# Performance work log

Measured on AMD Instinct MI355X. Metric: run time of the kernel, lower is better.

The kernel has to match this reference:

```python
import jax, jax.numpy as jnp
import numpy as np

N, E, IN_DIM, EMBED_DIM, HID_DIM = 10000, 320000, 128, 128, 64
NEG_SLOPE = 0.2


def setup_inputs() -> dict:
    key = jax.random.key(0)
    ks = jax.random.split(key, 7)
    x = jax.random.normal(ks[0], (N, IN_DIM), dtype=jnp.float32)
    edge_index = jax.random.randint(ks[1], (2, E), 0, N, dtype=jnp.int64)
    dense_w = jax.random.normal(ks[2], (IN_DIM, EMBED_DIM), dtype=jnp.float32) / np.sqrt(IN_DIM)
    dense_b = jnp.zeros((EMBED_DIM,), dtype=jnp.float32)
    gat_w = jax.random.normal(ks[3], (EMBED_DIM, HID_DIM), dtype=jnp.float32) / np.sqrt(EMBED_DIM)
    att_src = jax.random.normal(ks[4], (HID_DIM,), dtype=jnp.float32) * 0.1
    att_dst = jax.random.normal(ks[5], (HID_DIM,), dtype=jnp.float32) * 0.1
    gat_b = jnp.zeros((HID_DIM,), dtype=jnp.float32)
    return {"x": x, "edge_index": edge_index, "dense_w": dense_w, "dense_b": dense_b,
            "gat_w": gat_w, "att_src": att_src, "att_dst": att_dst, "gat_b": gat_b}


def reference(x, edge_index, dense_w, dense_b, gat_w, att_src, att_dst, gat_b):
    n = x.shape[0]
    # dense + relu
    h = jax.nn.relu(x @ dense_w + dense_b)            # [N, embed]
    # GATConv (heads=1): linear transform
    z = h @ gat_w                                     # [N, hid]
    # add self loops (PyG default)
    loops = jnp.arange(n, dtype=edge_index.dtype)
    src = jnp.concatenate([edge_index[0], loops])     # [E+N] message source j
    dst = jnp.concatenate([edge_index[1], loops])     # [E+N] message target i
    a_src = z @ att_src                               # [N]
    a_dst = z @ att_dst                               # [N]
    e = jax.nn.leaky_relu(a_src[src] + a_dst[dst], NEG_SLOPE)  # [E+N]
    # segment softmax over incoming edges of each target node
    m = jax.ops.segment_max(e, dst, num_segments=n)
    ex = jnp.exp(e - m[dst])
    denom = jax.ops.segment_sum(ex, dst, num_segments=n)
    alpha = ex / denom[dst]                           # [E+N]
    embed_x = jax.ops.segment_sum(alpha[:, None] * z[src], dst, num_segments=n) + gat_b  # [N, hid]
    # pairwise sigmoid similarity
    sim = jax.nn.sigmoid(embed_x @ embed_x.T)         # [N, N]
    return sim, embed_x
```

## Files before the change

kernel.cpp:

```cpp
#include <hip/hip_runtime.h>
#include <math.h>

#define N_NODES 10000
#define E_EDGES 320000
#define IN_DIM 128
#define EMB 128
#define HID 64
#define NEG_SLOPE 0.2f

typedef __attribute__((ext_vector_type(8))) short short8;
typedef __attribute__((ext_vector_type(4))) float floatx4;

__device__ __forceinline__ short f2bf(float f) {
    unsigned u = __float_as_uint(f);
    unsigned r = u + 0x7fffu + ((u >> 16) & 1u);
    return (short)(r >> 16);
}

__global__ __launch_bounds__(128) void dense_gat_kernel(
    const float* __restrict__ x, const float* __restrict__ dw,
    const float* __restrict__ db, const float* __restrict__ gw,
    const float* __restrict__ asv, const float* __restrict__ adv,
    float* __restrict__ z, float* __restrict__ a_src, float* __restrict__ a_dst)
{
    __shared__ float xs[8][IN_DIM];
    __shared__ float hs[8][EMB];
    const int t = threadIdx.x;
    const int row0 = blockIdx.x * 8;

    #pragma unroll
    for (int r = 0; r < 8; ++r)
        xs[r][t] = x[(row0 + r) * IN_DIM + t];
    __syncthreads();

    float acc[8];
    {
        const float bias = db[t];
        #pragma unroll
        for (int r = 0; r < 8; ++r) acc[r] = bias;
    }
    for (int j = 0; j < IN_DIM; ++j) {
        const float wj = dw[j * EMB + t];
        #pragma unroll
        for (int r = 0; r < 8; ++r) acc[r] = fmaf(xs[r][j], wj, acc[r]);
    }
    #pragma unroll
    for (int r = 0; r < 8; ++r) hs[r][t] = fmaxf(acc[r], 0.f);
    __syncthreads();

    if (t < HID) {
        float zacc[8];
        #pragma unroll
        for (int r = 0; r < 8; ++r) zacc[r] = 0.f;
        for (int k = 0; k < EMB; ++k) {
            const float g = gw[k * HID + t];
            #pragma unroll
            for (int r = 0; r < 8; ++r) zacc[r] = fmaf(hs[r][k], g, zacc[r]);
        }
        const float as = asv[t], ad = adv[t];
        #pragma unroll
        for (int r = 0; r < 8; ++r) {
            const int row = row0 + r;
            z[row * HID + t] = zacc[r];
            float ps = zacc[r] * as;
            float pd = zacc[r] * ad;
            #pragma unroll
            for (int off = 32; off > 0; off >>= 1) {
                ps += __shfl_down(ps, off, 64);
                pd += __shfl_down(pd, off, 64);
            }
            if (t == 0) { a_src[row] = ps; a_dst[row] = pd; }
        }
    }
}

__global__ __launch_bounds__(256) void count_kernel(
    const int* __restrict__ ei, int* __restrict__ cnt)
{
    const int e = blockIdx.x * blockDim.x + threadIdx.x;
    const int total = E_EDGES + N_NODES;
    if (e >= total) return;
    int s, d;
    if (e < E_EDGES) { s = ei[e]; d = ei[E_EDGES + e]; }
    else             { s = d = e - E_EDGES; }
    if ((unsigned)s >= N_NODES || (unsigned)d >= N_NODES) return;
    atomicAdd(&cnt[d], 1);
}

__global__ __launch_bounds__(256) void scan_kernel(
    const int* __restrict__ cnt, int* __restrict__ offs, int* __restrict__ cursor)
{
    __shared__ int part[256];
    const int t = threadIdx.x;
    const int base = t * 40;
    int vals[40];
    int local = 0;
    #pragma unroll
    for (int i = 0; i < 40; ++i) {
        const int idx = base + i;
        const int c = (idx < N_NODES) ? cnt[idx] : 0;
        vals[i] = c;
        local += c;
    }
    part[t] = local;
    __syncthreads();
    for (int off = 1; off < 256; off <<= 1) {
        const int v = (t >= off) ? part[t - off] : 0;
        __syncthreads();
        part[t] += v;
        __syncthreads();
    }
    int running = (t == 0) ? 0 : part[t - 1];
    #pragma unroll
    for (int i = 0; i < 40; ++i) {
        const int idx = base + i;
        if (idx < N_NODES) { offs[idx] = running; cursor[idx] = running; }
        running += vals[i];
    }
    if (t == 255) offs[N_NODES] = running;
}

__global__ __launch_bounds__(256) void scatter_kernel(
    const int* __restrict__ ei, const float* __restrict__ a_src,
    const float* __restrict__ a_dst, int* __restrict__ cursor,
    int* __restrict__ srcs, float* __restrict__ ew)
{
    const int e = blockIdx.x * blockDim.x + threadIdx.x;
    const int total = E_EDGES + N_NODES;
    if (e >= total) return;
    int s, d;
    if (e < E_EDGES) { s = ei[e]; d = ei[E_EDGES + e]; }
    else             { s = d = e - E_EDGES; }
    if ((unsigned)s >= N_NODES || (unsigned)d >= N_NODES) return;
    float v = a_src[s] + a_dst[d];
    v = (v > 0.f) ? v : NEG_SLOPE * v;
    const float w = __expf(v);
    const int pos = atomicAdd(&cursor[d], 1);
    srcs[pos] = s;
    ew[pos]   = w;
}

__global__ __launch_bounds__(256) void aggregate_kernel(
    const int* __restrict__ offs, const int* __restrict__ srcs,
    const float* __restrict__ ew, const float* __restrict__ z,
    const float* __restrict__ gb, float* __restrict__ emb)
{
    const int wid  = (blockIdx.x * blockDim.x + threadIdx.x) >> 6;
    const int lane = threadIdx.x & 63;
    if (wid >= N_NODES) return;
    const int beg = offs[wid], end = offs[wid + 1];
    float acc = 0.f, sw = 0.f;
    for (int i = beg; i < end; ++i) {
        const int s   = srcs[i];
        const float w = ew[i];
        acc = fmaf(w, z[s * HID + lane], acc);
        sw += w;
    }
    emb[wid * HID + lane] = acc / sw + gb[lane];
}

__global__ __launch_bounds__(256) void sim_kernel(
    const float* __restrict__ emb, float* __restrict__ sim)
{
    const int t    = threadIdx.x;
    const int lane = t & 63;
    const int wave = t >> 6;
    const int wm   = (wave >> 1) * 64;
    const int wn   = (wave & 1) * 64;
    const int rowBase = blockIdx.y * 128 + wm;
    const int colBase = blockIdx.x * 128 + wn;
    const int l15  = lane & 15;
    const int quad = lane >> 4;

    short8 afrag[4][2], bfrag[4][2];
    #pragma unroll
    for (int ti = 0; ti < 4; ++ti) {
        int r = rowBase + ti * 16 + l15; if (r > N_NODES - 1) r = N_NODES - 1;
        int c = colBase + ti * 16 + l15; if (c > N_NODES - 1) c = N_NODES - 1;
        #pragma unroll
        for (int ks = 0; ks < 2; ++ks) {
            const floatx4* pa = (const floatx4*)&emb[r * HID + ks * 32 + quad * 8];
            const floatx4* pb = (const floatx4*)&emb[c * HID + ks * 32 + quad * 8];
            const floatx4 a0 = pa[0], a1 = pa[1];
            const floatx4 b0 = pb[0], b1 = pb[1];
            short8 af, bf;
            #pragma unroll
            for (int j = 0; j < 4; ++j) { af[j] = f2bf(a0[j]); af[4 + j] = f2bf(a1[j]); }
            #pragma unroll
            for (int j = 0; j < 4; ++j) { bf[j] = f2bf(b0[j]); bf[4 + j] = f2bf(b1[j]); }
            afrag[ti][ks] = af;
            bfrag[ti][ks] = bf;
        }
    }

    floatx4 acc[4][4];
    const floatx4 zero = {0.f, 0.f, 0.f, 0.f};
    #pragma unroll
    for (int ti = 0; ti < 4; ++ti)
        #pragma unroll
        for (int tj = 0; tj < 4; ++tj) acc[ti][tj] = zero;

    #pragma unroll
    for (int ti = 0; ti < 4; ++ti)
        #pragma unroll
        for (int tj = 0; tj < 4; ++tj) {
            acc[ti][tj] = __builtin_amdgcn_mfma_f32_16x16x32_bf16(
                afrag[ti][0], bfrag[tj][0], acc[ti][tj], 0, 0, 0);
            acc[ti][tj] = __builtin_amdgcn_mfma_f32_16x16x32_bf16(
                afrag[ti][1], bfrag[tj][1], acc[ti][tj], 0, 0, 0);
        }

    #pragma unroll
    for (int ti = 0; ti < 4; ++ti) {
        #pragma unroll
        for (int reg = 0; reg < 4; ++reg) {
            const int gr = rowBase + ti * 16 + quad * 4 + reg;
            if (gr >= N_NODES) continue;
            const size_t rowoff = (size_t)gr * N_NODES;
            #pragma unroll
            for (int tj = 0; tj < 4; ++tj) {
                const int gc = colBase + tj * 16 + l15;
                if (gc < N_NODES) {
                    const float v = acc[ti][tj][reg];
                    sim[rowoff + gc] = __builtin_amdgcn_rcpf(1.f + __expf(-v));
                }
            }
        }
    }
}

extern "C" void kernel_launch(void* const* d_in, const int* in_sizes, int n_in,
                              void* d_out, int out_size, void* d_ws, size_t ws_size,
                              hipStream_t stream)
{
    const float* x   = (const float*)d_in[0];
    const int*   ei  = (const int*)d_in[1];
    const float* dw  = (const float*)d_in[2];
    const float* db  = (const float*)d_in[3];
    const float* gw  = (const float*)d_in[4];
    const float* asv = (const float*)d_in[5];
    const float* adv = (const float*)d_in[6];
    const float* gb  = (const float*)d_in[7];

    float* out = (float*)d_out;
    float* sim = out;
    float* emb = out + (size_t)N_NODES * N_NODES;

    const size_t need = 1350001u * sizeof(float);
    float* ws = (ws_size >= need) ? (float*)d_ws : out;
    float* z      = ws;
    float* a_src  = ws + 640000;
    float* a_dst  = ws + 650000;
    int*   cnt    = (int*)(ws + 660000);
    int*   offs   = (int*)(ws + 670000);
    int*   cursor = (int*)(ws + 680001);
    int*   srcs   = (int*)(ws + 690001);
    float* ew     = ws + 1020001;

    hipMemsetAsync(cnt, 0, N_NODES * sizeof(int), stream);

    dense_gat_kernel<<<N_NODES / 8, 128, 0, stream>>>(x, dw, db, gw, asv, adv,
                                                      z, a_src, a_dst);

    const int total_edges = E_EDGES + N_NODES;
    const int eb = (total_edges + 255) / 256;
    count_kernel<<<eb, 256, 0, stream>>>(ei, cnt);
    scan_kernel<<<1, 256, 0, stream>>>(cnt, offs, cursor);
    scatter_kernel<<<eb, 256, 0, stream>>>(ei, a_src, a_dst, cursor, srcs, ew);
    aggregate_kernel<<<(N_NODES * 64 + 255) / 256, 256, 0, stream>>>(
        offs, srcs, ew, z, gb, emb);

    dim3 grid((N_NODES + 127) / 128, (N_NODES + 127) / 128);
    sim_kernel<<<grid, 256, 0, stream>>>(emb, sim);
}
```

Baseline: 581.0 us.

## Stage sim tiles in LDS as bf16 and rebalance dense GAT kernel

Measured after the change: 563.3 us. 3.0% less time.

```diff
diff --git a/kernel.cpp b/kernel.cpp
--- a/kernel.cpp
+++ b/kernel.cpp
@@ -9,6 +9,7 @@
 #define NEG_SLOPE 0.2f
 
 typedef __attribute__((ext_vector_type(8))) short short8;
+typedef __attribute__((ext_vector_type(4))) short short4_t;
 typedef __attribute__((ext_vector_type(4))) float floatx4;
 
 __device__ __forceinline__ short f2bf(float f) {
@@ -17,61 +18,71 @@
     return (short)(r >> 16);
 }
 
-__global__ __launch_bounds__(128) void dense_gat_kernel(
+__global__ __launch_bounds__(256) void dense_gat_kernel(
     const float* __restrict__ x, const float* __restrict__ dw,
     const float* __restrict__ db, const float* __restrict__ gw,
-    const float* __restrict__ asv, const float* __restrict__ adv,
-    float* __restrict__ z, float* __restrict__ a_src, float* __restrict__ a_dst)
-{
-    __shared__ float xs[8][IN_DIM];
-    __shared__ float hs[8][EMB];
+    float* __restrict__ z)
+{
+    __shared__ float xs[16][IN_DIM];
+    __shared__ float hs[16][EMB];
     const int t = threadIdx.x;
-    const int row0 = blockIdx.x * 8;
-
-    #pragma unroll
-    for (int r = 0; r < 8; ++r)
-        xs[r][t] = x[(row0 + r) * IN_DIM + t];
-    __syncthreads();
-
-    float acc[8];
+    const int row0 = blockIdx.x * 16;
+
+    #pragma unroll
+    for (int r = 0; r < 2; ++r) {
+        const int idx = t + r * 256;
+        const int row = idx >> 5, c4 = idx & 31;
+        *(floatx4*)&xs[row][c4 * 4] =
+            *(const floatx4*)&x[(row0 + row) * IN_DIM + c4 * 4];
+    }
+    __syncthreads();
+
     {
-        const float bias = db[t];
+        const int col = t & 127, rb = (t >> 7) * 8;
+        float acc[8];
+        const float bias = db[col];
         #pragma unroll
         for (int r = 0; r < 8; ++r) acc[r] = bias;
-    }
-    for (int j = 0; j < IN_DIM; ++j) {
-        const float wj = dw[j * EMB + t];
-        #pragma unroll
-        for (int r = 0; r < 8; ++r) acc[r] = fmaf(xs[r][j], wj, acc[r]);
-    }
-    #pragma unroll
-    for (int r = 0; r < 8; ++r) hs[r][t] = fmaxf(acc[r], 0.f);
-    __syncthreads();
-
-    if (t < HID) {
-        float zacc[8];
-        #pragma unroll
-        for (int r = 0; r < 8; ++r) zacc[r] = 0.f;
+        for (int j = 0; j < IN_DIM; ++j) {
+            const float wj = dw[j * EMB + col];
+            #pragma unroll
+            for (int r = 0; r < 8; ++r) acc[r] = fmaf(xs[rb + r][j], wj, acc[r]);
+        }
+        #pragma unroll
+        for (int r = 0; r < 8; ++r) hs[rb + r][col] = fmaxf(acc[r], 0.f);
+    }
+    __syncthreads();
+
+    {
+        const int col = t & 63, rb = (t >> 6) * 4;
+        float acc[4] = {0.f, 0.f, 0.f, 0.f};
         for (int k = 0; k < EMB; ++k) {
-            const float g = gw[k * HID + t];
+            const float g = gw[k * HID + col];
             #pragma unroll
-            for (int r = 0; r < 8; ++r) zacc[r] = fmaf(hs[r][k], g, zacc[r]);
-        }
-        const float as = asv[t], ad = adv[t];
-        #pragma unroll
-        for (int r = 0; r < 8; ++r) {
-            const int row = row0 + r;
-            z[row * HID + t] = zacc[r];
-            float ps = zacc[r] * as;
-            float pd = zacc[r] * ad;
-            #pragma unroll
-            for (int off = 32; off > 0; off >>= 1) {
-                ps += __shfl_down(ps, off, 64);
-                pd += __shfl_down(pd, off, 64);
-            }
-            if (t == 0) { a_src[row] = ps; a_dst[row] = pd; }
-        }
-    }
+            for (int r = 0; r < 4; ++r) acc[r] = fmaf(hs[rb + r][k], g, acc[r]);
+        }
+        #pragma unroll
+        for (int r = 0; r < 4; ++r) z[(row0 + rb + r) * HID + col] = acc[r];
+    }
+}
+
+__global__ __launch_bounds__(256) void att_kernel(
+    const float* __restrict__ z, const float* __restrict__ asv,
+    const float* __restrict__ adv, float* __restrict__ a_src,
+    float* __restrict__ a_dst)
+{
+    const int wid  = (blockIdx.x * blockDim.x + threadIdx.x) >> 6;
+    const int lane = threadIdx.x & 63;
+    if (wid >= N_NODES) return;
+    const float zv = z[wid * HID + lane];
+    float ps = zv * asv[lane];
+    float pd = zv * adv[lane];
+    #pragma unroll
+    for (int off = 32; off > 0; off >>= 1) {
+        ps += __shfl_down(ps, off, 64);
+        pd += __shfl_down(pd, off, 64);
+    }
+    if (lane == 0) { a_src[wid] = ps; a_dst[wid] = pd; }
 }
 
 __global__ __launch_bounds__(256) void count_kernel(
@@ -159,39 +170,43 @@
     emb[wid * HID + lane] = acc / sw + gb[lane];
 }
 
+#define SROW 72
 __global__ __launch_bounds__(256) void sim_kernel(
     const float* __restrict__ emb, float* __restrict__ sim)
 {
+    __shared__ short As[128 * SROW];
+    __shared__ short Bs[128 * SROW];
     const int t    = threadIdx.x;
     const int lane = t & 63;
     const int wave = t >> 6;
     const int wm   = (wave >> 1) * 64;
     const int wn   = (wave & 1) * 64;
-    const int rowBase = blockIdx.y * 128 + wm;
-    const int colBase = blockIdx.x * 128 + wn;
     const int l15  = lane & 15;
     const int quad = lane >> 4;
 
-    short8 afrag[4][2], bfrag[4][2];
-    #pragma unroll
-    for (int ti = 0; ti < 4; ++ti) {
-        int r = rowBase + ti * 16 + l15; if (r > N_NODES - 1) r = N_NODES - 1;
-        int c = colBase + ti * 16 + l15; if (c > N_NODES - 1) c = N_NODES - 1;
-        #pragma unroll
-        for (int ks = 0; ks < 2; ++ks) {
-            const floatx4* pa = (const floatx4*)&emb[r * HID + ks * 32 + quad * 8];
-            const floatx4* pb = (const floatx4*)&emb[c * HID + ks * 32 + quad * 8];
-            const floatx4 a0 = pa[0], a1 = pa[1];
-            const floatx4 b0 = pb[0], b1 = pb[1];
-            short8 af, bf;
-            #pragma unroll
-            for (int j = 0; j < 4; ++j) { af[j] = f2bf(a0[j]); af[4 + j] = f2bf(a1[j]); }
-            #pragma unroll
-            for (int j = 0; j < 4; ++j) { bf[j] = f2bf(b0[j]); bf[4 + j] = f2bf(b1[j]); }
-            afrag[ti][ks] = af;
-            bfrag[ti][ks] = bf;
-        }
-    }
+    #pragma unroll
+    for (int round = 0; round < 8; ++round) {
+        const int idx = t + round * 256;
+        const int row = idx >> 4, c4 = idx & 15;
+        int gr = blockIdx.y * 128 + row; if (gr > N_NODES - 1) gr = N_NODES - 1;
+        int gc = blockIdx.x * 128 + row; if (gc > N_NODES - 1) gc = N_NODES - 1;
+        const floatx4 a = *(const floatx4*)&emb[gr * HID + c4 * 4];
+        const floatx4 b = *(const floatx4*)&emb[gc * HID + c4 * 4];
+        short4_t sa, sb;
+        #pragma unroll
+        for (int j = 0; j < 4; ++j) { sa[j] = f2bf(a[j]); sb[j] = f2bf(b[j]); }
+        *(short4_t*)&As[row * SROW + c4 * 4] = sa;
+        *(short4_t*)&Bs[row * SROW + c4 * 4] = sb;
+    }
+    __syncthreads();
+
+    short8 afrag[4][2];
+    #pragma unroll
+    for (int ti = 0; ti < 4; ++ti)
+        #pragma unroll
+        for (int ks = 0; ks < 2; ++ks)
+            afrag[ti][ks] = *(const short8*)&As[(wm + ti * 16 + l15) * SROW +
+                                                ks * 32 + quad * 8];
 
     floatx4 acc[4][4];
     const floatx4 zero = {0.f, 0.f, 0.f, 0.f};
@@ -201,25 +216,28 @@
         for (int tj = 0; tj < 4; ++tj) acc[ti][tj] = zero;
 
     #pragma unroll
-    for (int ti = 0; ti < 4; ++ti)
-        #pragma unroll
-        for (int tj = 0; tj < 4; ++tj) {
+    for (int tj = 0; tj < 4; ++tj) {
+        const short8 bf0 = *(const short8*)&Bs[(wn + tj * 16 + l15) * SROW + quad * 8];
+        const short8 bf1 = *(const short8*)&Bs[(wn + tj * 16 + l15) * SROW + 32 + quad * 8];
+        #pragma unroll
+        for (int ti = 0; ti < 4; ++ti) {
             acc[ti][tj] = __builtin_amdgcn_mfma_f32_16x16x32_bf16(
-                afrag[ti][0], bfrag[tj][0], acc[ti][tj], 0, 0, 0);
+                afrag[ti][0], bf0, acc[ti][tj], 0, 0, 0);
             acc[ti][tj] = __builtin_amdgcn_mfma_f32_16x16x32_bf16(
-                afrag[ti][1], bfrag[tj][1], acc[ti][tj], 0, 0, 0);
-        }
+                afrag[ti][1], bf1, acc[ti][tj], 0, 0, 0);
+        }
+    }
 
     #pragma unroll
     for (int ti = 0; ti < 4; ++ti) {
         #pragma unroll
         for (int reg = 0; reg < 4; ++reg) {
-            const int gr = rowBase + ti * 16 + quad * 4 + reg;
+            const int gr = blockIdx.y * 128 + wm + ti * 16 + quad * 4 + reg;
             if (gr >= N_NODES) continue;
             const size_t rowoff = (size_t)gr * N_NODES;
             #pragma unroll
             for (int tj = 0; tj < 4; ++tj) {
-                const int gc = colBase + tj * 16 + l15;
+                const int gc = blockIdx.x * 128 + wn + tj * 16 + l15;
                 if (gc < N_NODES) {
                     const float v = acc[ti][tj][reg];
                     sim[rowoff + gc] = __builtin_amdgcn_rcpf(1.f + __expf(-v));
@@ -259,8 +277,9 @@
 
     hipMemsetAsync(cnt, 0, N_NODES * sizeof(int), stream);
 
-    dense_gat_kernel<<<N_NODES / 8, 128, 0, stream>>>(x, dw, db, gw, asv, adv,
-                                                      z, a_src, a_dst);
+    dense_gat_kernel<<<N_NODES / 16, 256, 0, stream>>>(x, dw, db, gw, z);
+    att_kernel<<<(N_NODES * 64 + 255) / 256, 256, 0, stream>>>(z, asv, adv,
+                                                               a_src, a_dst);
 
     const int total_edges = E_EDGES + N_NODES;
     const int eb = (total_edges + 255) / 256;
```
